# Kernel optimization log

Hardware: AMD Instinct MI355X
Metric: run time of the kernel (lower is better)

Reference implementation:

```python
import jax, jax.numpy as jnp
import numpy as np


def setup_inputs() -> dict:
    key = jax.random.key(0)
    k1, k2 = jax.random.split(key)
    B, N, M = 2, 8192, 8192
    source_point_cloud = jax.random.normal(k1, (B, N, 3), dtype=jnp.float32)
    target_point_cloud = jax.random.normal(k2, (B, M, 3), dtype=jnp.float32)
    return {"source_point_cloud": source_point_cloud,
            "target_point_cloud": target_point_cloud}


def reference(source_point_cloud, target_point_cloud):
    # source: [B, N, 3], target: [B, M, 3]
    s, t = source_point_cloud, target_point_cloud
    # Brute-force exact 1-NN (replaces per-batch CPU cKDTree query).
    # ||s - t||^2 = ||s||^2 + ||t||^2 - 2 s.t ; argmin unaffected by const terms per row,
    # but keep ||t||^2 since it varies over the argmin axis.
    s2 = jnp.sum(s * s, axis=-1)                       # [B, N]
    t2 = jnp.sum(t * t, axis=-1)                       # [B, M]
    dots = jnp.einsum('bnd,bmd->bnm', s, t)            # [B, N, M]
    d2 = t2[:, None, :] - 2.0 * dots                   # [B, N, M] (drop s2: row-constant)
    idx = jnp.argmin(d2, axis=-1)                      # [B, N] nearest target index
    target_points = jnp.take_along_axis(t, idx[..., None], axis=1)  # [B, N, 3]
    # MSELoss (mean over all elements) per batch, then mean over batch.
    per_batch = jnp.mean((s - target_points) ** 2, axis=(1, 2))     # [B]
    return jnp.mean(per_batch)
```

## Files before the change

kernel.cpp:

```cpp
#include <hip/hip_runtime.h>

#define BLOCK  256
#define TSPLIT 32

typedef float vfloat2 __attribute__((ext_vector_type(2)));
typedef float vfloat4 __attribute__((ext_vector_type(4)));

__device__ __forceinline__ vfloat2 vlo(vfloat4 v) { return __builtin_shufflevector(v, v, 0, 1); }
__device__ __forceinline__ vfloat2 vhi(vfloat4 v) { return __builtin_shufflevector(v, v, 2, 3); }

__global__ __launch_bounds__(256) void prep_kernel(
    const float* __restrict__ tgt, float* __restrict__ soa,
    float* __restrict__ out, int M, int Mp, int BMp)
{
    int i = blockIdx.x * 256 + threadIdx.x;
    if (i == 0) out[0] = 0.f;
    if (i >= BMp) return;
    int b = i / Mp, m = i - b * Mp;
    float x = 0.f, y = 0.f, z = 0.f, w = 1e30f;
    if (m < M) {
        const float* p = tgt + ((size_t)b * M + m) * 3;
        x = p[0]; y = p[1]; z = p[2];
        w = fmaf(x, x, fmaf(y, y, z * z));
    }
    soa[i]           = x;
    soa[BMp + i]     = y;
    soa[2 * BMp + i] = z;
    soa[3 * BMp + i] = w;
}

__global__ __launch_bounds__(BLOCK, 8) void nn_chunk_kernel(
    const float* __restrict__ src, const float* __restrict__ soa,
    float* __restrict__ partial, int N, int Mp, int BMp, int SGB, int BN)
{
    const int tid = threadIdx.x;
    const int c   = blockIdx.x % TSPLIT;
    const int sgg = blockIdx.x / TSPLIT;
    const int b   = sgg / SGB;
    const int sgl = sgg - b * SGB;
    const int si  = sgl * BLOCK + tid;

    float x = 0.f, y = 0.f, z = 0.f;
    if (si < N) {
        const float* p = src + ((size_t)b * N + si) * 3;
        x = p[0]; y = p[1]; z = p[2];
    }
    const vfloat2 nsx = {-2.f * x, -2.f * x};
    const vfloat2 nsy = {-2.f * y, -2.f * y};
    const vfloat2 nsz = {-2.f * z, -2.f * z};
    float mind = 1e30f;

    const int CHT = Mp / TSPLIT;
    const int f4  = (b * Mp + c * CHT) >> 2;
    const vfloat4* __restrict__ TX = (const vfloat4*)soa;
    const vfloat4* __restrict__ TY = (const vfloat4*)(soa + BMp);
    const vfloat4* __restrict__ TZ = (const vfloat4*)(soa + 2 * BMp);
    const vfloat4* __restrict__ TW = (const vfloat4*)(soa + 3 * BMp);

#pragma unroll 2
    for (int k = 0; k < CHT / 8; ++k) {
        vfloat4 xa = TX[f4 + 2 * k], xb = TX[f4 + 2 * k + 1];
        vfloat4 ya = TY[f4 + 2 * k], yb = TY[f4 + 2 * k + 1];
        vfloat4 za = TZ[f4 + 2 * k], zb = TZ[f4 + 2 * k + 1];
        vfloat4 wa = TW[f4 + 2 * k], wb = TW[f4 + 2 * k + 1];

        vfloat2 d;
        d = __builtin_elementwise_fma(vlo(xa), nsx, vlo(wa));
        d = __builtin_elementwise_fma(vlo(ya), nsy, d);
        d = __builtin_elementwise_fma(vlo(za), nsz, d);
        mind = fminf(mind, fminf(d.x, d.y));

        d = __builtin_elementwise_fma(vhi(xa), nsx, vhi(wa));
        d = __builtin_elementwise_fma(vhi(ya), nsy, d);
        d = __builtin_elementwise_fma(vhi(za), nsz, d);
        mind = fminf(mind, fminf(d.x, d.y));

        d = __builtin_elementwise_fma(vlo(xb), nsx, vlo(wb));
        d = __builtin_elementwise_fma(vlo(yb), nsy, d);
        d = __builtin_elementwise_fma(vlo(zb), nsz, d);
        mind = fminf(mind, fminf(d.x, d.y));

        d = __builtin_elementwise_fma(vhi(xb), nsx, vhi(wb));
        d = __builtin_elementwise_fma(vhi(yb), nsy, d);
        d = __builtin_elementwise_fma(vhi(zb), nsz, d);
        mind = fminf(mind, fminf(d.x, d.y));
    }

    if (si < N) {
        partial[(size_t)c * BN + (size_t)b * N + si] = mind;
    }
}

__global__ __launch_bounds__(BLOCK) void reduce_kernel(
    const float* __restrict__ src, const float* __restrict__ partial,
    float* __restrict__ out, int BN, float scale)
{
    const int i = blockIdx.x * BLOCK + threadIdx.x;
    float v = 0.f;
    if (i < BN) {
        float m0 = 1e30f, m1 = 1e30f, m2 = 1e30f, m3 = 1e30f;
#pragma unroll
        for (int c = 0; c < TSPLIT; c += 4) {
            m0 = fminf(m0, partial[(size_t)(c + 0) * BN + i]);
            m1 = fminf(m1, partial[(size_t)(c + 1) * BN + i]);
            m2 = fminf(m2, partial[(size_t)(c + 2) * BN + i]);
            m3 = fminf(m3, partial[(size_t)(c + 3) * BN + i]);
        }
        float x = src[(size_t)i * 3 + 0];
        float y = src[(size_t)i * 3 + 1];
        float z = src[(size_t)i * 3 + 2];
        v = fmaf(x, x, fmaf(y, y, z * z))
          + fminf(fminf(m0, m1), fminf(m2, m3));
    }

#pragma unroll
    for (int off = 32; off > 0; off >>= 1) v += __shfl_xor(v, off, 64);

    __shared__ float wsum[BLOCK / 64];
    const int lane = threadIdx.x & 63;
    const int w    = threadIdx.x >> 6;
    if (lane == 0) wsum[w] = v;
    __syncthreads();
    if (threadIdx.x == 0) {
        float s = 0.f;
#pragma unroll
        for (int k = 0; k < BLOCK / 64; ++k) s += wsum[k];
        atomicAdd(out, s * scale);
    }
}

extern "C" void kernel_launch(void* const* d_in, const int* in_sizes, int n_in,
                              void* d_out, int out_size, void* d_ws, size_t ws_size,
                              hipStream_t stream) {
    const float* src = (const float*)d_in[0];
    const float* tgt = (const float*)d_in[1];
    float* out = (float*)d_out;

    const int B = 2;
    const int N = in_sizes[0] / (B * 3);
    const int M = in_sizes[1] / (B * 3);
    const int BN = B * N;

    const int step = TSPLIT * 8;
    const int Mp  = ((M + step - 1) / step) * step;
    const int BMp = B * Mp;

    float* soa     = (float*)d_ws;
    float* partial = soa + 4 * (size_t)BMp;

    prep_kernel<<<(BMp + 255) / 256, 256, 0, stream>>>(tgt, soa, out, M, Mp, BMp);

    const int SGB = (N + BLOCK - 1) / BLOCK;
    const int grid1 = B * SGB * TSPLIT;
    nn_chunk_kernel<<<grid1, BLOCK, 0, stream>>>(src, soa, partial,
                                                 N, Mp, BMp, SGB, BN);

    reduce_kernel<<<(BN + BLOCK - 1) / BLOCK, BLOCK, 0, stream>>>(
        src, partial, out, BN, 1.0f / (3.0f * (float)N * (float)B));
}
```

Measured before the change: 73.13 us.

## Fuse final reduction into NN kernel via atomicMin keys and last-block sum

Drops the separate reduce kernel and the partial-min buffer. Each thread now atomically mins an order-preserving integer key of its full squared distance into a per-source buffer. A grid-wide counter then lets the last finishing block sum all minima and write the loss. This removes one launch and the partial write/read traffic. In exchange it adds global atomics per thread, a threadfence per block, and a serial final sum done by a single block.

```diff
diff --git a/kernel.cpp b/kernel.cpp
--- a/kernel.cpp
+++ b/kernel.cpp
@@ -9,12 +9,23 @@
 __device__ __forceinline__ vfloat2 vlo(vfloat4 v) { return __builtin_shufflevector(v, v, 0, 1); }
 __device__ __forceinline__ vfloat2 vhi(vfloat4 v) { return __builtin_shufflevector(v, v, 2, 3); }
 
+__device__ __forceinline__ unsigned fkey(float f) {
+    unsigned b = __float_as_uint(f);
+    return b ^ ((unsigned)((int)b >> 31) | 0x80000000u);
+}
+__device__ __forceinline__ float funkey(unsigned k) {
+    unsigned b = (k & 0x80000000u) ? (k ^ 0x80000000u) : ~k;
+    return __uint_as_float(b);
+}
+
 __global__ __launch_bounds__(256) void prep_kernel(
     const float* __restrict__ tgt, float* __restrict__ soa,
-    float* __restrict__ out, int M, int Mp, int BMp)
+    unsigned* __restrict__ minbuf, unsigned* __restrict__ counter,
+    int M, int Mp, int BMp, int BN)
 {
     int i = blockIdx.x * 256 + threadIdx.x;
-    if (i == 0) out[0] = 0.f;
+    if (i == 0) *counter = 0u;
+    if (i < BN) minbuf[i] = 0xFFFFFFFFu;
     if (i >= BMp) return;
     int b = i / Mp, m = i - b * Mp;
     float x = 0.f, y = 0.f, z = 0.f, w = 1e30f;
@@ -31,7 +42,9 @@
 
 __global__ __launch_bounds__(BLOCK, 8) void nn_chunk_kernel(
     const float* __restrict__ src, const float* __restrict__ soa,
-    float* __restrict__ partial, int N, int Mp, int BMp, int SGB, int BN)
+    unsigned* __restrict__ minbuf, unsigned* __restrict__ counter,
+    float* __restrict__ out, int N, int Mp, int BMp, int SGB, int BN,
+    float scale)
 {
     const int tid = threadIdx.x;
     const int c   = blockIdx.x % TSPLIT;
@@ -87,45 +100,38 @@
     }
 
     if (si < N) {
-        partial[(size_t)c * BN + (size_t)b * N + si] = mind;
-    }
-}
-
-__global__ __launch_bounds__(BLOCK) void reduce_kernel(
-    const float* __restrict__ src, const float* __restrict__ partial,
-    float* __restrict__ out, int BN, float scale)
-{
-    const int i = blockIdx.x * BLOCK + threadIdx.x;
-    float v = 0.f;
-    if (i < BN) {
-        float m0 = 1e30f, m1 = 1e30f, m2 = 1e30f, m3 = 1e30f;
-#pragma unroll
-        for (int c = 0; c < TSPLIT; c += 4) {
-            m0 = fminf(m0, partial[(size_t)(c + 0) * BN + i]);
-            m1 = fminf(m1, partial[(size_t)(c + 1) * BN + i]);
-            m2 = fminf(m2, partial[(size_t)(c + 2) * BN + i]);
-            m3 = fminf(m3, partial[(size_t)(c + 3) * BN + i]);
-        }
-        float x = src[(size_t)i * 3 + 0];
-        float y = src[(size_t)i * 3 + 1];
-        float z = src[(size_t)i * 3 + 2];
-        v = fmaf(x, x, fmaf(y, y, z * z))
-          + fminf(fminf(m0, m1), fminf(m2, m3));
+        float f = fmaf(x, x, fmaf(y, y, z * z)) + mind;
+        atomicMin(&minbuf[b * N + si], fkey(f));
     }
 
+    __threadfence();
+    __shared__ int is_last;
+    if (tid == 0) {
+        unsigned done = atomicAdd(counter, 1u);
+        is_last = (done == (unsigned)(gridDim.x - 1)) ? 1 : 0;
+    }
+    __syncthreads();
+    if (is_last) {
+        __threadfence();
+        float s = 0.f;
+        for (int j = tid; j < BN; j += BLOCK) {
+            unsigned k = __hip_atomic_load(&minbuf[j], __ATOMIC_RELAXED,
+                                           __HIP_MEMORY_SCOPE_AGENT);
+            s += funkey(k);
+        }
 #pragma unroll
-    for (int off = 32; off > 0; off >>= 1) v += __shfl_xor(v, off, 64);
-
-    __shared__ float wsum[BLOCK / 64];
-    const int lane = threadIdx.x & 63;
-    const int w    = threadIdx.x >> 6;
-    if (lane == 0) wsum[w] = v;
-    __syncthreads();
-    if (threadIdx.x == 0) {
-        float s = 0.f;
+        for (int off = 32; off > 0; off >>= 1) s += __shfl_xor(s, off, 64);
+        __shared__ float wsum[BLOCK / 64];
+        const int lane = tid & 63;
+        const int w    = tid >> 6;
+        if (lane == 0) wsum[w] = s;
+        __syncthreads();
+        if (tid == 0) {
+            float t = 0.f;
 #pragma unroll
-        for (int k = 0; k < BLOCK / 64; ++k) s += wsum[k];
-        atomicAdd(out, s * scale);
+            for (int k2 = 0; k2 < BLOCK / 64; ++k2) t += wsum[k2];
+            out[0] = t * scale;
+        }
     }
 }
 
@@ -145,16 +151,17 @@
     const int Mp  = ((M + step - 1) / step) * step;
     const int BMp = B * Mp;
 
-    float* soa     = (float*)d_ws;
-    float* partial = soa + 4 * (size_t)BMp;
+    unsigned* counter = (unsigned*)d_ws;
+    unsigned* minbuf  = counter + 64;
+    float*    soa     = (float*)(minbuf + BN);
 
-    prep_kernel<<<(BMp + 255) / 256, 256, 0, stream>>>(tgt, soa, out, M, Mp, BMp);
+    int prep_n = (BMp > BN ? BMp : BN);
+    prep_kernel<<<(prep_n + 255) / 256, 256, 0, stream>>>(
+        tgt, soa, minbuf, counter, M, Mp, BMp, BN);
 
     const int SGB = (N + BLOCK - 1) / BLOCK;
     const int grid1 = B * SGB * TSPLIT;
-    nn_chunk_kernel<<<grid1, BLOCK, 0, stream>>>(src, soa, partial,
-                                                 N, Mp, BMp, SGB, BN);
-
-    reduce_kernel<<<(BN + BLOCK - 1) / BLOCK, BLOCK, 0, stream>>>(
-        src, partial, out, BN, 1.0f / (3.0f * (float)N * (float)B));
+    nn_chunk_kernel<<<grid1, BLOCK, 0, stream>>>(
+        src, soa, minbuf, counter, out, N, Mp, BMp, SGB, BN,
+        1.0f / (3.0f * (float)N * (float)B));
 }
```

New measurement: 198.5 us. 2.71x slower.
